# Optimization experiments

Hardware: AMD Instinct MI355X
Metric: run time of the kernel (lower is better)

Reference implementation:

```python
import jax, jax.numpy as jnp
import numpy as np

GLOBAL = 3
BETA = 10
CR, CO, CS = 9, 2, 1
N_PCA = 45
PARENTS = [0, 1, 2, 0, 4, 5, 0, 7, 8, 0, 10, 11, 0, 13, 14]
JOINT_REORDER_MESH = {4: 743, 8: 333, 12: 443, 16: 555, 20: 678}


def rodrigues(r):
    # r: [..., 3] axis-angle -> [..., 3, 3] rotation matrix
    theta = jnp.sqrt(jnp.sum(r * r, axis=-1, keepdims=True) + 1e-8)
    n = r / theta
    th = theta[..., None]
    c, s = jnp.cos(th), jnp.sin(th)
    nx, ny, nz = n[..., 0], n[..., 1], n[..., 2]
    z = jnp.zeros_like(nx)
    K = jnp.stack([z, -nz, ny, nz, z, -nx, -ny, nx, z], axis=-1).reshape(r.shape[:-1] + (3, 3))
    outer = n[..., :, None] * n[..., None, :]
    eye = jnp.eye(3, dtype=r.dtype)
    return c * eye + (1.0 - c) * outer + s * K


def setup_inputs() -> dict:
    key = jax.random.key(0)
    ks = jax.random.split(key, 12)
    B, T, D = 32, 128, 5376
    out_dim = N_PCA + GLOBAL + BETA + CR + CO + CS  # 70
    return {
        "x": jax.random.normal(ks[0], (B, T, D), dtype=jnp.float32),
        "W": jax.random.normal(ks[1], (out_dim, D), dtype=jnp.float32) * 0.01,
        "b": jax.random.normal(ks[2], (out_dim,), dtype=jnp.float32) * 0.01,
        "hand_ppal_comps": jax.random.normal(ks[3], (N_PCA, 45), dtype=jnp.float32) * 0.1,
        "mean_hand": jax.random.normal(ks[4], (45,), dtype=jnp.float32) * 0.1,
        "hand_template": jax.random.normal(ks[5], (778, 3), dtype=jnp.float32) * 0.05,
        "shapedirs": jax.random.normal(ks[6], (778, 3, 10), dtype=jnp.float32) * 0.01,
        "posedirs": jax.random.normal(ks[7], (778, 3, 135), dtype=jnp.float32) * 0.01,
        "J_reg": jax.random.uniform(ks[8], (16, 778), dtype=jnp.float32) / 778.0,
        "lbs_weights": jax.nn.softmax(jax.random.normal(ks[9], (778, 16), dtype=jnp.float32), axis=-1),
    }


def _forward(x, W, b, hand_ppal_comps, mean_hand, hand_template, shapedirs, posedirs, J_reg, lbs_weights):
    N, T, _ = x.shape
    params = x @ W.T + b  # [N,T,70]
    n_pca = hand_ppal_comps.shape[0]
    off = GLOBAL + n_pca
    theta = params[..., :off]
    beta = params[..., off:off + BETA]
    c_r = params[..., off + BETA:off + BETA + CR]
    c_o = params[..., off + BETA + CR:off + BETA + CR + CO]
    c_s = params[..., off + BETA + CR + CO:off + BETA + CR + CO + CS]

    # pose from PCA
    hand_posed = theta[..., GLOBAL:] @ hand_ppal_comps + mean_hand  # [N,T,45]
    hand_posed = jnp.concatenate([theta[..., :GLOBAL], hand_posed], axis=-1)  # [N,T,48]

    # shape blendshapes and joints
    hand_shaped = jnp.einsum('vck,btk->btvc', shapedirs, beta) + hand_template  # [N,T,778,3]
    J = jnp.einsum('jv,btvc->btjc', J_reg, hand_shaped)  # [N,T,16,3]

    # pose blendshapes (lrotmin: flattened Rodrigues matrices of the 15 finger joints)
    rod135 = rodrigues(hand_posed[..., GLOBAL:].reshape(N, T, 15, 3)).reshape(N, T, 135)
    curr_hand = hand_shaped + jnp.einsum('vck,btk->btvc', posedirs, rod135)

    # global rigid transformation (kinematic tree)
    rot16 = rodrigues(hand_posed.reshape(N, T, 16, 3))  # [N,T,16,3,3]
    row = jnp.broadcast_to(jnp.array([0.0, 0.0, 0.0, 1.0], dtype=x.dtype), (N, T, 1, 4))
    T0 = jnp.concatenate([jnp.concatenate([rot16[:, :, 0], J[:, :, 0, :, None]], axis=-1), row], axis=-2)  # [N,T,4,4]
    parents = np.array(PARENTS)
    rel = (J[:, :, 1:] - J[:, :, parents])[..., None]  # [N,T,15,3,1]
    op = jnp.concatenate([rot16[:, :, 1:], rel], axis=-1)  # [N,T,15,3,4]
    row15 = jnp.broadcast_to(jnp.array([0.0, 0.0, 0.0, 1.0], dtype=x.dtype), (N, T, 15, 1, 4))
    op = jnp.concatenate([op, row15], axis=-2)  # [N,T,15,4,4]
    res = [T0]
    for i in range(15):
        res.append(res[PARENTS[i]] @ op[:, :, i])
    results = jnp.stack(res, axis=2)  # [N,T,16,4,4]

    ext_J = jnp.concatenate([J, jnp.zeros((N, T, 16, 1), dtype=x.dtype)], axis=-1)
    corr = jnp.einsum('btjik,btjk->btji', results, ext_J)  # [N,T,16,4]
    A = results - jnp.concatenate([jnp.zeros((N, T, 16, 4, 3), dtype=x.dtype), corr[..., None]], axis=-1)
    J3d = results[..., :3, 3]  # [N,T,16,3]

    # linear blend skinning
    Tv = jnp.einsum('btjik,vj->btvik', A, lbs_weights)  # [N,T,778,4,4]
    curr_h = jnp.concatenate([curr_hand, jnp.ones((N, T, 778, 1), dtype=x.dtype)], axis=-1)
    mesh = jnp.einsum('btvij,btvj->btvi', Tv, curr_h)[..., :3]  # [N,T,778,3]

    jr = lambda i: J3d[:, :, i]
    mv = lambda v: mesh[:, :, v]
    J3d_re = jnp.stack([jr(0), jr(13), jr(14), jr(15), mv(743), jr(1), jr(2), jr(3), mv(333),
                        jr(4), jr(5), jr(6), mv(443), jr(10), jr(11), jr(12), mv(555),
                        jr(7), jr(8), jr(9), mv(678)], axis=2)  # [N,T,21,3]

    c_r3 = c_r.reshape(N, T, 3, 3)
    J2d = (J3d_re @ c_r3)[..., :2]
    J2d = c_s[:, :, None] * J2d + c_o[:, :, None]
    return (J2d, theta, beta)


def reference(x, W, b, hand_ppal_comps, mean_hand, hand_template, shapedirs, posedirs, J_reg, lbs_weights):
    return _forward(x, W, b, hand_ppal_comps, mean_hand, hand_template, shapedirs, posedirs, J_reg, lbs_weights)
```

## Files before the change

kernel.cpp:

```cpp
#include <hip/hip_runtime.h>
#include <hip/hip_bf16.h>

typedef short short8 __attribute__((ext_vector_type(8)));
typedef float float4_ __attribute__((ext_vector_type(4)));
typedef unsigned short ushort_t;

#define OUT_THETA 172032
#define OUT_BETA  368640
#define NROW 4096
#define KDIM 5376
#define NPAD 80
#define KS 21
#define BK 128

__device__ __constant__ int c_jslot[16] = {0,5,6,7,9,10,11,17,18,19,13,14,15,1,2,3};
__device__ __constant__ int c_vslot[5]  = {4,8,12,16,20};

__device__ inline short f2bf(float f) {
  union { float f; unsigned u; } v; v.f = f;
  unsigned r = v.u + 0x7fffu + ((v.u >> 16) & 1u);
  return (short)(r >> 16);
}

__device__ inline short8 cvt8(float4_ a, float4_ b) {
  short8 r;
  r[0]=f2bf(a[0]); r[1]=f2bf(a[1]); r[2]=f2bf(a[2]); r[3]=f2bf(a[3]);
  r[4]=f2bf(b[0]); r[5]=f2bf(b[1]); r[6]=f2bf(b[2]); r[7]=f2bf(b[3]);
  return r;
}

__global__ __launch_bounds__(256) void setup_kernel(
    const float* __restrict__ W, const float* __restrict__ shapedirs,
    const float* __restrict__ posedirs, const float* __restrict__ Jreg,
    const float* __restrict__ tmpl, const float* __restrict__ lbs,
    ushort_t* __restrict__ wfrag, float* __restrict__ jsd, float* __restrict__ jt,
    float* __restrict__ psel, float* __restrict__ ssel, float* __restrict__ tsel,
    float* __restrict__ wsel)
{
  int b = blockIdx.x, t = threadIdx.x;
  if (b < 210) {
    int idx = b*256 + t;
    int n = idx / 672, kg = idx % 672;
    short8 o;
    if (n < 70) {
      const float* wp = W + (size_t)n*KDIM + kg*8;
      float4_ w0 = *(const float4_*)wp;
      float4_ w1 = *(const float4_*)(wp+4);
      o = cvt8(w0, w1);
    } else {
      o = (short8){0,0,0,0,0,0,0,0};
    }
    *(short8*)(wfrag + ((size_t)kg*NPAD + n)*8) = o;
  } else if (b < 342) {
    int wv = (b-210)*4 + (t>>6);
    int l = t & 63;
    float p = 0.f;
    if (wv < 480) {
      int j = wv/30, r = wv%30, c = r/10, kk = r%10;
      for (int v = l; v < 778; v += 64) p += Jreg[j*778+v]*shapedirs[(v*3+c)*10+kk];
    } else {
      int o = wv-480; int j = o/3, c = o%3;
      for (int v = l; v < 778; v += 64) p += Jreg[j*778+v]*tmpl[v*3+c];
    }
    for (int off = 32; off > 0; off >>= 1) p += __shfl_down(p, off);
    if (l == 0) { if (wv < 480) jsd[wv] = p; else jt[wv-480] = p; }
  } else {
    const int vtx[5] = {743,333,443,555,678};
    for (int s = t; s < 2270; s += 256) {
      if (s < 2025) { int vi = s/405, r = s%405, c = r/135, kk = r%135;
        psel[s] = posedirs[((size_t)vtx[vi]*3 + c)*135 + kk]; }
      else if (s < 2175) { int u = s-2025; int vi = u/30, r = u%30, c = r/10, kk = r%10;
        ssel[u] = shapedirs[((size_t)vtx[vi]*3 + c)*10 + kk]; }
      else if (s < 2190) { int u = s-2175; int vi = u/3, c = u%3;
        tsel[u] = tmpl[vtx[vi]*3 + c]; }
      else if (s < 2270) { int u = s-2190; int vi = u/16, j = u%16;
        wsel[u] = lbs[vtx[vi]*16 + j]; }
    }
  }
}

__global__ __launch_bounds__(256) void gemm_params(
    const float* __restrict__ x, const ushort_t* __restrict__ wfrag,
    float* __restrict__ part)
{
  __shared__ float As[64*BK];
  int t = threadIdx.x;
  int rb = blockIdx.x & 63;
  int kq = blockIdx.x >> 6;
  int m_base = rb << 6;
  int k0 = kq * 256;

  int l = t & 63, w = t >> 6;
  int q = l >> 4, lm = l & 15;
  int r = w*16 + lm;
  int sw = r & 7;

  float4_ acc0 = {0.f,0.f,0.f,0.f}, acc1 = acc0, acc2 = acc0, acc3 = acc0, acc4 = acc0;
  const float4_* As4 = (const float4_*)As;

  #pragma unroll
  for (int it = 0; it < 2; ++it) {
    #pragma unroll
    for (int j = 0; j < 8; ++j) {
      int f = j*256 + t;
      int row = f >> 5, p = f & 31;
      int g = p ^ (row & 7);
      const float* src = x + (size_t)(m_base + row)*KDIM + k0 + it*BK + g*4;
      __builtin_amdgcn_global_load_lds(
          (const __attribute__((address_space(1))) void*)src,
          (__attribute__((address_space(3))) void*)&As[(size_t)f*4], 16, 0, 0);
    }
    __syncthreads();

    #pragma unroll
    for (int c = 0; c < 4; ++c) {
      int cc = it*4 + c;
      int Lg = c*8 + q*2;
      float4_ f0 = As4[r*32 + (Lg ^ sw)];
      float4_ f1 = As4[r*32 + ((Lg+1) ^ sw)];
      const ushort_t* bp = wfrag + ((size_t)((k0>>3) + cc*4 + q)*NPAD + lm)*8;
      short8 b0 = *(const short8*)(bp);
      short8 b1 = *(const short8*)(bp+128);
      short8 b2 = *(const short8*)(bp+256);
      short8 b3 = *(const short8*)(bp+384);
      short8 b4 = *(const short8*)(bp+512);
      short8 af = cvt8(f0, f1);
      acc0 = __builtin_amdgcn_mfma_f32_16x16x32_bf16(af, b0, acc0, 0, 0, 0);
      acc1 = __builtin_amdgcn_mfma_f32_16x16x32_bf16(af, b1, acc1, 0, 0, 0);
      acc2 = __builtin_amdgcn_mfma_f32_16x16x32_bf16(af, b2, acc2, 0, 0, 0);
      acc3 = __builtin_amdgcn_mfma_f32_16x16x32_bf16(af, b3, acc3, 0, 0, 0);
      acc4 = __builtin_amdgcn_mfma_f32_16x16x32_bf16(af, b4, acc4, 0, 0, 0);
    }
    __syncthreads();
  }

  float* op = part + ((size_t)kq*NROW + m_base + w*16 + q*4)*NPAD + lm;
  #pragma unroll
  for (int rr = 0; rr < 4; ++rr) {
    op[(size_t)rr*NPAD +  0] = acc0[rr];
    op[(size_t)rr*NPAD + 16] = acc1[rr];
    op[(size_t)rr*NPAD + 32] = acc2[rr];
    op[(size_t)rr*NPAD + 48] = acc3[rr];
    op[(size_t)rr*NPAD + 64] = acc4[rr];
  }
}

__global__ __launch_bounds__(64) void decode_kernel(
    const float* __restrict__ part, const float* __restrict__ bvec,
    const float* __restrict__ comps, const float* __restrict__ meanh,
    const float* __restrict__ jsd, const float* __restrict__ jt,
    const float* __restrict__ psel, const float* __restrict__ ssel,
    const float* __restrict__ tsel, const float* __restrict__ wsel,
    float* __restrict__ out)
{
  int row = blockIdx.x;
  int l = threadIdx.x;
  __shared__ float P[70];
  __shared__ float HP[48];
  __shared__ float R[16][9];
  __shared__ float Jl[48];
  __shared__ float RES[16][16];
  __shared__ float Al[16][16];
  __shared__ float CH[5][4];
  __shared__ float M3[21][3];

  {
    float v = bvec[l];
    #pragma unroll
    for (int k = 0; k < KS; ++k) v += part[((size_t)k*NROW + row)*NPAD + l];
    P[l] = v;
    if (l < 48) out[OUT_THETA + (size_t)row*48 + l] = v;
    else if (l < 58) out[OUT_BETA + (size_t)row*10 + (l-48)] = v;
    if (l < 6) {
      int c2 = l + 64;
      float w = bvec[c2];
      #pragma unroll
      for (int k = 0; k < KS; ++k) w += part[((size_t)k*NROW + row)*NPAD + c2];
      P[c2] = w;
    }
  }
  __syncthreads();

  if (l < 45) {
    float s = meanh[l];
    for (int k = 0; k < 45; ++k) s += P[3+k]*comps[k*45 + l];
    HP[3+l] = s;
  } else if (l < 48) HP[l-45] = P[l-45];
  __syncthreads();

  if (l < 16) {
    float rx = HP[3*l], ry = HP[3*l+1], rz = HP[3*l+2];
    float th = sqrtf(rx*rx + ry*ry + rz*rz + 1e-8f);
    float inv = 1.0f/th;
    float nx = rx*inv, ny = ry*inv, nz = rz*inv;
    float cth = cosf(th), sth = sinf(th), mc = 1.0f - cth;
    R[l][0] = cth + mc*nx*nx;     R[l][1] = mc*nx*ny - sth*nz;  R[l][2] = mc*nx*nz + sth*ny;
    R[l][3] = mc*ny*nx + sth*nz;  R[l][4] = cth + mc*ny*ny;     R[l][5] = mc*ny*nz - sth*nx;
    R[l][6] = mc*nz*nx - sth*ny;  R[l][7] = mc*nz*ny + sth*nx;  R[l][8] = cth + mc*nz*nz;
  }
  if (l < 48) {
    float s = jt[l];
    #pragma unroll
    for (int k = 0; k < 10; ++k) s += jsd[l*10+k]*P[48+k];
    Jl[l] = s;
  }
  __syncthreads();

  if (l < 16) {
    int r = l >> 2, c = l & 3;
    RES[0][l] = (r < 3) ? ((c < 3) ? R[0][3*r+c] : Jl[r]) : ((c == 3) ? 1.f : 0.f);
  }
  __syncthreads();
  constexpr int PARS[15] = {0,1,2,0,4,5,0,7,8,0,10,11,0,13,14};
  #pragma unroll
  for (int i = 0; i < 15; ++i) {
    const int p = PARS[i];
    if (l < 16) {
      int r = l >> 2, c = l & 3;
      float s = (c == 3) ? RES[p][4*r+3] : 0.f;
      #pragma unroll
      for (int k = 0; k < 3; ++k) {
        float opv = (c < 3) ? R[i+1][3*k+c] : (Jl[3*(i+1)+k] - Jl[3*p+k]);
        s += RES[p][4*r+k]*opv;
      }
      RES[i+1][l] = s;
    }
    __syncthreads();
  }

  {
    int j = l >> 2, r = l & 3;
    float corr = RES[j][4*r]*Jl[3*j] + RES[j][4*r+1]*Jl[3*j+1] + RES[j][4*r+2]*Jl[3*j+2];
    Al[j][4*r+0] = RES[j][4*r+0];
    Al[j][4*r+1] = RES[j][4*r+1];
    Al[j][4*r+2] = RES[j][4*r+2];
    Al[j][4*r+3] = RES[j][4*r+3] - corr;
  }
  if (l < 15) {
    int vi = l/3, ci = l%3;
    float s = tsel[l];
    #pragma unroll
    for (int k = 0; k < 10; ++k) s += ssel[l*10+k]*P[48+k];
    for (int j15 = 0; j15 < 15; ++j15) {
      #pragma unroll
      for (int e = 0; e < 9; ++e) s += psel[l*135 + j15*9 + e]*R[j15+1][e];
    }
    CH[vi][ci] = s;
  }
  __syncthreads();

  if (l < 48) {
    int j = l/3, c = l%3;
    M3[c_jslot[j]][c] = RES[j][4*c+3];
  } else if (l < 63) {
    int s0 = l - 48; int vi = s0/3, r = s0%3;
    float m = 0.f;
    #pragma unroll
    for (int j = 0; j < 16; ++j) {
      float tv = Al[j][4*r]*CH[vi][0] + Al[j][4*r+1]*CH[vi][1]
               + Al[j][4*r+2]*CH[vi][2] + Al[j][4*r+3];
      m += wsel[vi*16+j]*tv;
    }
    M3[c_vslot[vi]][r] = m;
  }
  __syncthreads();

  if (l < 42) {
    int k = l >> 1, d = l & 1;
    float s = M3[k][0]*P[58 + d] + M3[k][1]*P[58 + 3 + d] + M3[k][2]*P[58 + 6 + d];
    out[((size_t)row*21 + k)*2 + d] = P[69]*s + P[67+d];
  }
}

extern "C" void kernel_launch(void* const* d_in, const int* in_sizes, int n_in,
                              void* d_out, int out_size, void* d_ws, size_t ws_size,
                              hipStream_t stream) {
  const float* x         = (const float*)d_in[0];
  const float* W         = (const float*)d_in[1];
  const float* bvec      = (const float*)d_in[2];
  const float* comps     = (const float*)d_in[3];
  const float* meanh     = (const float*)d_in[4];
  const float* tmpl      = (const float*)d_in[5];
  const float* shapedirs = (const float*)d_in[6];
  const float* posedirs  = (const float*)d_in[7];
  const float* Jreg      = (const float*)d_in[8];
  const float* lbs       = (const float*)d_in[9];

  const size_t PART_ONE = (size_t)NROW*NPAD*4;

  char* ws = (char*)d_ws;
  float*    part  = (float*)ws;
  ushort_t* wfrag = (ushort_t*)(ws + (size_t)KS*PART_ONE);
  char*     tb    = ws + (size_t)KS*PART_ONE + 860160;
  float* jsd  = (float*)tb;
  float* jt   = (float*)(tb + 1920);
  float* psel = (float*)(tb + 1920 + 192);
  float* ssel = (float*)(tb + 1920 + 192 + 8100);
  float* tsel = (float*)(tb + 1920 + 192 + 8100 + 600);
  float* wsel = (float*)(tb + 1920 + 192 + 8100 + 600 + 60);
  float* out  = (float*)d_out;

  hipLaunchKernelGGL(setup_kernel, dim3(343), dim3(256), 0, stream,
                     W, shapedirs, posedirs, Jreg, tmpl, lbs,
                     wfrag, jsd, jt, psel, ssel, tsel, wsel);
  hipLaunchKernelGGL(gemm_params, dim3(64*KS), dim3(256), 0, stream,
                     x, wfrag, part);
  hipLaunchKernelGGL(decode_kernel, dim3(4096), dim3(64), 0, stream,
                     part, bvec, comps, meanh, jsd, jt, psel, ssel, tsel, wsel, out);
}
```

Before: 183.3 us.

## Fuse setup, GEMM and decode into one cooperative persistent kernel

Merges the three launches into a single cooperative kernel of 448 blocks that uses grid-wide syncs between the setup, GEMM and decode phases. The split-K factor drops from 21 to 14, and each block now computes two K-chunks of three BK tiles each. Decode runs per wavefront over three passes of rows using shared-memory slices. The aim is to remove launch gaps and cut partial-sum traffic, at the cost of grid sync overhead, fewer GEMM blocks in flight and a serial decode loop per wave.

```diff
diff --git a/kernel.cpp b/kernel.cpp
--- a/kernel.cpp
+++ b/kernel.cpp
@@ -1,5 +1,8 @@
 #include <hip/hip_runtime.h>
 #include <hip/hip_bf16.h>
+#include <hip/hip_cooperative_groups.h>
+
+namespace cg = cooperative_groups;
 
 typedef short short8 __attribute__((ext_vector_type(8)));
 typedef float float4_ __attribute__((ext_vector_type(4)));
@@ -10,8 +13,19 @@
 #define NROW 4096
 #define KDIM 5376
 #define NPAD 80
-#define KS 21
+#define KS 14
 #define BK 128
+#define NBLK 448
+
+#define DP_P    0
+#define DP_HP   70
+#define DP_R    118
+#define DP_JL   262
+#define DP_RES  310
+#define DP_AL   566
+#define DP_CH   822
+#define DP_M3   842
+#define DP_STRIDE 912
 
 __device__ __constant__ int c_jslot[16] = {0,5,6,7,9,10,11,17,18,19,13,14,15,1,2,3};
 __device__ __constant__ int c_vslot[5]  = {4,8,12,16,20};
@@ -29,18 +43,149 @@
   return r;
 }
 
-__global__ __launch_bounds__(256) void setup_kernel(
-    const float* __restrict__ W, const float* __restrict__ shapedirs,
-    const float* __restrict__ posedirs, const float* __restrict__ Jreg,
-    const float* __restrict__ tmpl, const float* __restrict__ lbs,
+__device__ void decode_item(float* D, int row, int l, bool valid,
+    const float* __restrict__ part, const float* __restrict__ bvec,
+    const float* __restrict__ comps, const float* __restrict__ meanh,
+    const float* __restrict__ jsd, const float* __restrict__ jt,
+    const float* __restrict__ psel, const float* __restrict__ ssel,
+    const float* __restrict__ tsel, const float* __restrict__ wsel,
+    float* __restrict__ out)
+{
+  if (valid) {
+    float v = bvec[l];
+    #pragma unroll
+    for (int k = 0; k < KS; ++k) v += part[((size_t)k*NROW + row)*NPAD + l];
+    D[DP_P + l] = v;
+    if (l < 48) out[OUT_THETA + (size_t)row*48 + l] = v;
+    else if (l < 58) out[OUT_BETA + (size_t)row*10 + (l-48)] = v;
+    if (l < 6) {
+      int c2 = l + 64;
+      float w = bvec[c2];
+      #pragma unroll
+      for (int k = 0; k < KS; ++k) w += part[((size_t)k*NROW + row)*NPAD + c2];
+      D[DP_P + c2] = w;
+    }
+  } else {
+    D[DP_P + l] = 0.f;
+    if (l < 6) D[DP_P + 64 + l] = 0.f;
+  }
+  __syncthreads();
+
+  if (l < 45) {
+    float s = meanh[l];
+    for (int k = 0; k < 45; ++k) s += D[DP_P + 3 + k]*comps[k*45 + l];
+    D[DP_HP + 3 + l] = s;
+  } else if (l < 48) D[DP_HP + (l-45)] = D[DP_P + (l-45)];
+  __syncthreads();
+
+  if (l < 16) {
+    float rx = D[DP_HP + 3*l], ry = D[DP_HP + 3*l+1], rz = D[DP_HP + 3*l+2];
+    float th = sqrtf(rx*rx + ry*ry + rz*rz + 1e-8f);
+    float inv = 1.0f/th;
+    float nx = rx*inv, ny = ry*inv, nz = rz*inv;
+    float cth = cosf(th), sth = sinf(th), mc = 1.0f - cth;
+    float* R = D + DP_R + 9*l;
+    R[0] = cth + mc*nx*nx;     R[1] = mc*nx*ny - sth*nz;  R[2] = mc*nx*nz + sth*ny;
+    R[3] = mc*ny*nx + sth*nz;  R[4] = cth + mc*ny*ny;     R[5] = mc*ny*nz - sth*nx;
+    R[6] = mc*nz*nx - sth*ny;  R[7] = mc*nz*ny + sth*nx;  R[8] = cth + mc*nz*nz;
+  }
+  if (l < 48) {
+    float s = jt[l];
+    #pragma unroll
+    for (int k = 0; k < 10; ++k) s += jsd[l*10+k]*D[DP_P + 48 + k];
+    D[DP_JL + l] = s;
+  }
+  __syncthreads();
+
+  if (l < 16) {
+    int r = l >> 2, c = l & 3;
+    D[DP_RES + l] = (r < 3) ? ((c < 3) ? D[DP_R + 3*r + c] : D[DP_JL + r])
+                            : ((c == 3) ? 1.f : 0.f);
+  }
+  __syncthreads();
+  constexpr int PARS[15] = {0,1,2,0,4,5,0,7,8,0,10,11,0,13,14};
+  #pragma unroll
+  for (int i = 0; i < 15; ++i) {
+    const int p = PARS[i];
+    if (l < 16) {
+      int r = l >> 2, c = l & 3;
+      float s = (c == 3) ? D[DP_RES + p*16 + 4*r + 3] : 0.f;
+      #pragma unroll
+      for (int k = 0; k < 3; ++k) {
+        float opv = (c < 3) ? D[DP_R + (i+1)*9 + 3*k + c]
+                            : (D[DP_JL + 3*(i+1) + k] - D[DP_JL + 3*p + k]);
+        s += D[DP_RES + p*16 + 4*r + k]*opv;
+      }
+      D[DP_RES + (i+1)*16 + l] = s;
+    }
+    __syncthreads();
+  }
+
+  {
+    int j = l >> 2, r = l & 3;
+    const float* RS = D + DP_RES + j*16 + 4*r;
+    float corr = RS[0]*D[DP_JL+3*j] + RS[1]*D[DP_JL+3*j+1] + RS[2]*D[DP_JL+3*j+2];
+    float* AL = D + DP_AL + j*16 + 4*r;
+    AL[0] = RS[0]; AL[1] = RS[1]; AL[2] = RS[2]; AL[3] = RS[3] - corr;
+  }
+  if (l < 15) {
+    int vi = l/3, ci = l%3;
+    float s = tsel[l];
+    #pragma unroll
+    for (int k = 0; k < 10; ++k) s += ssel[l*10+k]*D[DP_P + 48 + k];
+    for (int j15 = 0; j15 < 15; ++j15) {
+      #pragma unroll
+      for (int e = 0; e < 9; ++e) s += psel[l*135 + j15*9 + e]*D[DP_R + (j15+1)*9 + e];
+    }
+    D[DP_CH + vi*4 + ci] = s;
+  }
+  __syncthreads();
+
+  if (l < 48) {
+    int j = l/3, c = l%3;
+    D[DP_M3 + c_jslot[j]*3 + c] = D[DP_RES + j*16 + 4*c + 3];
+  } else if (l < 63) {
+    int s0 = l - 48; int vi = s0/3, r = s0%3;
+    float m = 0.f;
+    #pragma unroll
+    for (int j = 0; j < 16; ++j) {
+      const float* AL = D + DP_AL + j*16 + 4*r;
+      float tv = AL[0]*D[DP_CH+vi*4] + AL[1]*D[DP_CH+vi*4+1]
+               + AL[2]*D[DP_CH+vi*4+2] + AL[3];
+      m += wsel[vi*16+j]*tv;
+    }
+    D[DP_M3 + c_vslot[vi]*3 + r] = m;
+  }
+  __syncthreads();
+
+  if (valid && l < 42) {
+    int k = l >> 1, d = l & 1;
+    float s = D[DP_M3+k*3]*D[DP_P+58+d] + D[DP_M3+k*3+1]*D[DP_P+58+3+d]
+            + D[DP_M3+k*3+2]*D[DP_P+58+6+d];
+    out[((size_t)row*21 + k)*2 + d] = D[DP_P+69]*s + D[DP_P+67+d];
+  }
+  __syncthreads();
+}
+
+__global__ __launch_bounds__(256, 2) void fused_kernel(
+    const float* __restrict__ x, const float* __restrict__ W,
+    const float* __restrict__ bvec, const float* __restrict__ comps,
+    const float* __restrict__ meanh, const float* __restrict__ tmpl,
+    const float* __restrict__ shapedirs, const float* __restrict__ posedirs,
+    const float* __restrict__ Jreg, const float* __restrict__ lbs,
     ushort_t* __restrict__ wfrag, float* __restrict__ jsd, float* __restrict__ jt,
     float* __restrict__ psel, float* __restrict__ ssel, float* __restrict__ tsel,
-    float* __restrict__ wsel)
+    float* __restrict__ wsel, float* __restrict__ part, float* __restrict__ out)
 {
-  int b = blockIdx.x, t = threadIdx.x;
-  if (b < 210) {
-    int idx = b*256 + t;
-    int n = idx / 672, kg = idx % 672;
+  __shared__ float LB[8192];
+  cg::grid_group grid = cg::this_grid();
+  int t = threadIdx.x;
+  int gid = blockIdx.x*256 + t;
+  int gw = gid >> 6;
+  int l = t & 63, w = t >> 6;
+
+  if (gw < 840) {
+    int n = gid / 672, kg = gid % 672;
     short8 o;
     if (n < 70) {
       const float* wp = W + (size_t)n*KDIM + kg*8;
@@ -51,9 +196,8 @@
       o = (short8){0,0,0,0,0,0,0,0};
     }
     *(short8*)(wfrag + ((size_t)kg*NPAD + n)*8) = o;
-  } else if (b < 342) {
-    int wv = (b-210)*4 + (t>>6);
-    int l = t & 63;
+  } else if (gw < 1368) {
+    int wv = gw - 840;
     float p = 0.f;
     if (wv < 480) {
       int j = wv/30, r = wv%30, c = r/10, kk = r%10;
@@ -64,211 +208,96 @@
     }
     for (int off = 32; off > 0; off >>= 1) p += __shfl_down(p, off);
     if (l == 0) { if (wv < 480) jsd[wv] = p; else jt[wv-480] = p; }
-  } else {
+  } else if (gid >= 87552 && gid < 87552 + 2270) {
     const int vtx[5] = {743,333,443,555,678};
-    for (int s = t; s < 2270; s += 256) {
-      if (s < 2025) { int vi = s/405, r = s%405, c = r/135, kk = r%135;
-        psel[s] = posedirs[((size_t)vtx[vi]*3 + c)*135 + kk]; }
-      else if (s < 2175) { int u = s-2025; int vi = u/30, r = u%30, c = r/10, kk = r%10;
-        ssel[u] = shapedirs[((size_t)vtx[vi]*3 + c)*10 + kk]; }
-      else if (s < 2190) { int u = s-2175; int vi = u/3, c = u%3;
-        tsel[u] = tmpl[vtx[vi]*3 + c]; }
-      else if (s < 2270) { int u = s-2190; int vi = u/16, j = u%16;
-        wsel[u] = lbs[vtx[vi]*16 + j]; }
-    }
-  }
-}
-
-__global__ __launch_bounds__(256) void gemm_params(
-    const float* __restrict__ x, const ushort_t* __restrict__ wfrag,
-    float* __restrict__ part)
-{
-  __shared__ float As[64*BK];
-  int t = threadIdx.x;
-  int rb = blockIdx.x & 63;
-  int kq = blockIdx.x >> 6;
-  int m_base = rb << 6;
-  int k0 = kq * 256;
-
-  int l = t & 63, w = t >> 6;
-  int q = l >> 4, lm = l & 15;
-  int r = w*16 + lm;
-  int sw = r & 7;
-
-  float4_ acc0 = {0.f,0.f,0.f,0.f}, acc1 = acc0, acc2 = acc0, acc3 = acc0, acc4 = acc0;
-  const float4_* As4 = (const float4_*)As;
-
-  #pragma unroll
-  for (int it = 0; it < 2; ++it) {
-    #pragma unroll
-    for (int j = 0; j < 8; ++j) {
-      int f = j*256 + t;
-      int row = f >> 5, p = f & 31;
-      int g = p ^ (row & 7);
-      const float* src = x + (size_t)(m_base + row)*KDIM + k0 + it*BK + g*4;
-      __builtin_amdgcn_global_load_lds(
-          (const __attribute__((address_space(1))) void*)src,
-          (__attribute__((address_space(3))) void*)&As[(size_t)f*4], 16, 0, 0);
-    }
-    __syncthreads();
-
-    #pragma unroll
-    for (int c = 0; c < 4; ++c) {
-      int cc = it*4 + c;
-      int Lg = c*8 + q*2;
-      float4_ f0 = As4[r*32 + (Lg ^ sw)];
-      float4_ f1 = As4[r*32 + ((Lg+1) ^ sw)];
-      const ushort_t* bp = wfrag + ((size_t)((k0>>3) + cc*4 + q)*NPAD + lm)*8;
-      short8 b0 = *(const short8*)(bp);
-      short8 b1 = *(const short8*)(bp+128);
-      short8 b2 = *(const short8*)(bp+256);
-      short8 b3 = *(const short8*)(bp+384);
-      short8 b4 = *(const short8*)(bp+512);
-      short8 af = cvt8(f0, f1);
-      acc0 = __builtin_amdgcn_mfma_f32_16x16x32_bf16(af, b0, acc0, 0, 0, 0);
-      acc1 = __builtin_amdgcn_mfma_f32_16x16x32_bf16(af, b1, acc1, 0, 0, 0);
-      acc2 = __builtin_amdgcn_mfma_f32_16x16x32_bf16(af, b2, acc2, 0, 0, 0);
-      acc3 = __builtin_amdgcn_mfma_f32_16x16x32_bf16(af, b3, acc3, 0, 0, 0);
-      acc4 = __builtin_amdgcn_mfma_f32_16x16x32_bf16(af, b4, acc4, 0, 0, 0);
-    }
-    __syncthreads();
-  }
-
-  float* op = part + ((size_t)kq*NROW + m_base + w*16 + q*4)*NPAD + lm;
-  #pragma unroll
-  for (int rr = 0; rr < 4; ++rr) {
-    op[(size_t)rr*NPAD +  0] = acc0[rr];
-    op[(size_t)rr*NPAD + 16] = acc1[rr];
-    op[(size_t)rr*NPAD + 32] = acc2[rr];
-    op[(size_t)rr*NPAD + 48] = acc3[rr];
-    op[(size_t)rr*NPAD + 64] = acc4[rr];
-  }
-}
-
-__global__ __launch_bounds__(64) void decode_kernel(
-    const float* __restrict__ part, const float* __restrict__ bvec,
-    const float* __restrict__ comps, const float* __restrict__ meanh,
-    const float* __restrict__ jsd, const float* __restrict__ jt,
-    const float* __restrict__ psel, const float* __restrict__ ssel,
-    const float* __restrict__ tsel, const float* __restrict__ wsel,
-    float* __restrict__ out)
-{
-  int row = blockIdx.x;
-  int l = threadIdx.x;
-  __shared__ float P[70];
-  __shared__ float HP[48];
-  __shared__ float R[16][9];
-  __shared__ float Jl[48];
-  __shared__ float RES[16][16];
-  __shared__ float Al[16][16];
-  __shared__ float CH[5][4];
-  __shared__ float M3[21][3];
+    int s = gid - 87552;
+    if (s < 2025) { int vi = s/405, r = s%405, c = r/135, kk = r%135;
+      psel[s] = posedirs[((size_t)vtx[vi]*3 + c)*135 + kk]; }
+    else if (s < 2175) { int u = s-2025; int vi = u/30, r = u%30, c = r/10, kk = r%10;
+      ssel[u] = shapedirs[((size_t)vtx[vi]*3 + c)*10 + kk]; }
+    else if (s < 2190) { int u = s-2175; int vi = u/3, c = u%3;
+      tsel[u] = tmpl[vtx[vi]*3 + c]; }
+    else { int u = s-2190; int vi = u/16, j = u%16;
+      wsel[u] = lbs[vtx[vi]*16 + j]; }
+  }
+
+  grid.sync();
 
   {
-    float v = bvec[l];
-    #pragma unroll
-    for (int k = 0; k < KS; ++k) v += part[((size_t)k*NROW + row)*NPAD + l];
-    P[l] = v;
-    if (l < 48) out[OUT_THETA + (size_t)row*48 + l] = v;
-    else if (l < 58) out[OUT_BETA + (size_t)row*10 + (l-48)] = v;
-    if (l < 6) {
-      int c2 = l + 64;
-      float w = bvec[c2];
-      #pragma unroll
-      for (int k = 0; k < KS; ++k) w += part[((size_t)k*NROW + row)*NPAD + c2];
-      P[c2] = w;
-    }
-  }
-  __syncthreads();
-
-  if (l < 45) {
-    float s = meanh[l];
-    for (int k = 0; k < 45; ++k) s += P[3+k]*comps[k*45 + l];
-    HP[3+l] = s;
-  } else if (l < 48) HP[l-45] = P[l-45];
-  __syncthreads();
-
-  if (l < 16) {
-    float rx = HP[3*l], ry = HP[3*l+1], rz = HP[3*l+2];
-    float th = sqrtf(rx*rx + ry*ry + rz*rz + 1e-8f);
-    float inv = 1.0f/th;
-    float nx = rx*inv, ny = ry*inv, nz = rz*inv;
-    float cth = cosf(th), sth = sinf(th), mc = 1.0f - cth;
-    R[l][0] = cth + mc*nx*nx;     R[l][1] = mc*nx*ny - sth*nz;  R[l][2] = mc*nx*nz + sth*ny;
-    R[l][3] = mc*ny*nx + sth*nz;  R[l][4] = cth + mc*ny*ny;     R[l][5] = mc*ny*nz - sth*nx;
-    R[l][6] = mc*nz*nx - sth*ny;  R[l][7] = mc*nz*ny + sth*nx;  R[l][8] = cth + mc*nz*nz;
-  }
-  if (l < 48) {
-    float s = jt[l];
-    #pragma unroll
-    for (int k = 0; k < 10; ++k) s += jsd[l*10+k]*P[48+k];
-    Jl[l] = s;
-  }
-  __syncthreads();
-
-  if (l < 16) {
-    int r = l >> 2, c = l & 3;
-    RES[0][l] = (r < 3) ? ((c < 3) ? R[0][3*r+c] : Jl[r]) : ((c == 3) ? 1.f : 0.f);
-  }
-  __syncthreads();
-  constexpr int PARS[15] = {0,1,2,0,4,5,0,7,8,0,10,11,0,13,14};
-  #pragma unroll
-  for (int i = 0; i < 15; ++i) {
-    const int p = PARS[i];
-    if (l < 16) {
-      int r = l >> 2, c = l & 3;
-      float s = (c == 3) ? RES[p][4*r+3] : 0.f;
-      #pragma unroll
-      for (int k = 0; k < 3; ++k) {
-        float opv = (c < 3) ? R[i+1][3*k+c] : (Jl[3*(i+1)+k] - Jl[3*p+k]);
-        s += RES[p][4*r+k]*opv;
+    float* As = LB;
+    int rb = blockIdx.x & 63;
+    int m_base = rb << 6;
+    int q = l >> 4, lm = l & 15;
+    int r = w*16 + lm;
+    int sw = r & 7;
+    const float4_* As4 = (const float4_*)As;
+
+    #pragma unroll
+    for (int half = 0; half < 2; ++half) {
+      int kq = (blockIdx.x >> 6) + half*7;
+      int k0 = kq * (3*BK);
+
+      float4_ acc0 = {0.f,0.f,0.f,0.f}, acc1 = acc0, acc2 = acc0, acc3 = acc0, acc4 = acc0;
+
+      #pragma unroll
+      for (int it = 0; it < 3; ++it) {
+        #pragma unroll
+        for (int j = 0; j < 8; ++j) {
+          int f = j*256 + t;
+          int row = f >> 5, p = f & 31;
+          int g = p ^ (row & 7);
+          const float* src = x + (size_t)(m_base + row)*KDIM + k0 + it*BK + g*4;
+          __builtin_amdgcn_global_load_lds(
+              (const __attribute__((address_space(1))) void*)src,
+              (__attribute__((address_space(3))) void*)&As[(size_t)f*4], 16, 0, 0);
+        }
+        __syncthreads();
+
+        #pragma unroll
+        for (int c = 0; c < 4; ++c) {
+          int cc = it*4 + c;
+          int Lg = c*8 + q*2;
+          float4_ f0 = As4[r*32 + (Lg ^ sw)];
+          float4_ f1 = As4[r*32 + ((Lg+1) ^ sw)];
+          const ushort_t* bp = wfrag + ((size_t)((k0>>3) + cc*4 + q)*NPAD + lm)*8;
+          short8 b0 = *(const short8*)(bp);
+          short8 b1 = *(const short8*)(bp+128);
+          short8 b2 = *(const short8*)(bp+256);
+          short8 b3 = *(const short8*)(bp+384);
+          short8 b4 = *(const short8*)(bp+512);
+          short8 af = cvt8(f0, f1);
+          acc0 = __builtin_amdgcn_mfma_f32_16x16x32_bf16(af, b0, acc0, 0, 0, 0);
+          acc1 = __builtin_amdgcn_mfma_f32_16x16x32_bf16(af, b1, acc1, 0, 0, 0);
+          acc2 = __builtin_amdgcn_mfma_f32_16x16x32_bf16(af, b2, acc2, 0, 0, 0);
+          acc3 = __builtin_amdgcn_mfma_f32_16x16x32_bf16(af, b3, acc3, 0, 0, 0);
+          acc4 = __builtin_amdgcn_mfma_f32_16x16x32_bf16(af, b4, acc4, 0, 0, 0);
+        }
+        __syncthreads();
       }
-      RES[i+1][l] = s;
-    }
-    __syncthreads();
-  }
+
+      float* op = part + ((size_t)kq*NROW + m_base + w*16 + q*4)*NPAD + lm;
+      #pragma unroll
+      for (int rr = 0; rr < 4; ++rr) {
+        op[(size_t)rr*NPAD +  0] = acc0[rr];
+        op[(size_t)rr*NPAD + 16] = acc1[rr];
+        op[(size_t)rr*NPAD + 32] = acc2[rr];
+        op[(size_t)rr*NPAD + 48] = acc3[rr];
+        op[(size_t)rr*NPAD + 64] = acc4[rr];
+      }
+    }
+  }
+
+  grid.sync();
 
   {
-    int j = l >> 2, r = l & 3;
-    float corr = RES[j][4*r]*Jl[3*j] + RES[j][4*r+1]*Jl[3*j+1] + RES[j][4*r+2]*Jl[3*j+2];
-    Al[j][4*r+0] = RES[j][4*r+0];
-    Al[j][4*r+1] = RES[j][4*r+1];
-    Al[j][4*r+2] = RES[j][4*r+2];
-    Al[j][4*r+3] = RES[j][4*r+3] - corr;
-  }
-  if (l < 15) {
-    int vi = l/3, ci = l%3;
-    float s = tsel[l];
-    #pragma unroll
-    for (int k = 0; k < 10; ++k) s += ssel[l*10+k]*P[48+k];
-    for (int j15 = 0; j15 < 15; ++j15) {
-      #pragma unroll
-      for (int e = 0; e < 9; ++e) s += psel[l*135 + j15*9 + e]*R[j15+1][e];
-    }
-    CH[vi][ci] = s;
-  }
-  __syncthreads();
-
-  if (l < 48) {
-    int j = l/3, c = l%3;
-    M3[c_jslot[j]][c] = RES[j][4*c+3];
-  } else if (l < 63) {
-    int s0 = l - 48; int vi = s0/3, r = s0%3;
-    float m = 0.f;
-    #pragma unroll
-    for (int j = 0; j < 16; ++j) {
-      float tv = Al[j][4*r]*CH[vi][0] + Al[j][4*r+1]*CH[vi][1]
-               + Al[j][4*r+2]*CH[vi][2] + Al[j][4*r+3];
-      m += wsel[vi*16+j]*tv;
-    }
-    M3[c_vslot[vi]][r] = m;
-  }
-  __syncthreads();
-
-  if (l < 42) {
-    int k = l >> 1, d = l & 1;
-    float s = M3[k][0]*P[58 + d] + M3[k][1]*P[58 + 3 + d] + M3[k][2]*P[58 + 6 + d];
-    out[((size_t)row*21 + k)*2 + d] = P[69]*s + P[67+d];
+    float* D = LB + w*DP_STRIDE;
+    int wg = blockIdx.x*4 + w;
+    #pragma unroll
+    for (int pass = 0; pass < 3; ++pass) {
+      int row = wg + pass*1792;
+      decode_item(D, row, l, row < NROW,
+                  part, bvec, comps, meanh, jsd, jt, psel, ssel, tsel, wsel, out);
+    }
   }
 }
 
@@ -300,11 +329,9 @@
   float* wsel = (float*)(tb + 1920 + 192 + 8100 + 600 + 60);
   float* out  = (float*)d_out;
 
-  hipLaunchKernelGGL(setup_kernel, dim3(343), dim3(256), 0, stream,
-                     W, shapedirs, posedirs, Jreg, tmpl, lbs,
-                     wfrag, jsd, jt, psel, ssel, tsel, wsel);
-  hipLaunchKernelGGL(gemm_params, dim3(64*KS), dim3(256), 0, stream,
-                     x, wfrag, part);
-  hipLaunchKernelGGL(decode_kernel, dim3(4096), dim3(64), 0, stream,
-                     part, bvec, comps, meanh, jsd, jt, psel, ssel, tsel, wsel, out);
-}
+  void* args[] = { &x, &W, &bvec, &comps, &meanh, &tmpl, &shapedirs, &posedirs,
+                   &Jreg, &lbs, &wfrag, &jsd, &jt, &psel, &ssel, &tsel, &wsel,
+                   &part, &out };
+  hipLaunchCooperativeKernel((const void*)fused_kernel, dim3(NBLK), dim3(256),
+                             args, 0, stream);
+}
```

Measured after the change: 328.6 us. 1.79x slower.
